# Performance work log

Measured on AMD Instinct MI355X. Metric: run time of the kernel, lower is better.

The kernel has to match this reference:

```python
import jax, jax.numpy as jnp
import numpy as np

D = 1024
H = 16
HD = D // H
T = 2048
B = 2
EPS = 1e-7

def setup_inputs() -> dict:
    key = jax.random.key(0)
    ks = jax.random.split(key, 16)
    s = 0.02
    return {
        "x":  jax.random.normal(ks[0], (B, T, D), jnp.float32),
        "Wq": jax.random.normal(ks[1], (D, D), jnp.float32) * s,
        "bq": jnp.zeros((D,), jnp.float32),
        "Wk": jax.random.normal(ks[2], (D, D), jnp.float32) * s,
        "bk": jnp.zeros((D,), jnp.float32),
        "Wv": jax.random.normal(ks[3], (D, D), jnp.float32) * s,
        "bv": jnp.zeros((D,), jnp.float32),
        "Wo": jax.random.normal(ks[4], (D, D), jnp.float32) * s,
        "bo": jnp.zeros((D,), jnp.float32),
        "W1": jax.random.normal(ks[5], (D, 4 * D), jnp.float32) * s,
        "b1": jnp.zeros((4 * D,), jnp.float32),
        "W2": jax.random.normal(ks[6], (4 * D, D), jnp.float32) * s,
        "b2": jnp.zeros((D,), jnp.float32),
        "g1": jnp.ones((D,), jnp.float32),
        "be1": jnp.zeros((D,), jnp.float32),
        "g2": jnp.ones((D,), jnp.float32),
        "be2": jnp.zeros((D,), jnp.float32),
    }

def layer_norm(x, gamma, beta):
    mu = jnp.mean(x, axis=-1, keepdims=True)
    var = jnp.mean(jnp.square(x - mu), axis=-1, keepdims=True)  # biased var
    return (x - mu) / jnp.sqrt(var + EPS) * gamma + beta

def attention(x, Wq, bq, Wk, bk, Wv, bv, Wo, bo):
    b, t, d = x.shape
    q = (x @ Wq + bq).reshape(b, t, H, HD).transpose(0, 2, 1, 3)  # [B,H,T,HD]
    k = (x @ Wk + bk).reshape(b, t, H, HD).transpose(0, 2, 1, 3)
    v = (x @ Wv + bv).reshape(b, t, H, HD).transpose(0, 2, 1, 3)
    scores = jnp.einsum("bhqd,bhkd->bhqk", q, k) / np.sqrt(HD).astype(np.float32)
    causal = jnp.tril(jnp.ones((t, t), bool))
    scores = jnp.where(causal, scores, -jnp.inf)
    attn = jax.nn.softmax(scores, axis=-1)
    out = jnp.einsum("bhqk,bhkd->bhqd", attn, v)
    out = out.transpose(0, 2, 1, 3).reshape(b, t, d)
    return out @ Wo + bo

def reference(x, Wq, bq, Wk, bk, Wv, bv, Wo, bo, W1, b1, W2, b2, g1, be1, g2, be2):
    x = x + attention(layer_norm(x, g1, be1), Wq, bq, Wk, bk, Wv, bv, Wo, bo)
    h = layer_norm(x, g2, be2)
    x = x + (jax.nn.relu(h @ W1 + b1) @ W2 + b2)
    return x
```

## Files before the change

kernel.cpp:

```cpp
#include <hip/hip_runtime.h>
#include <hip/hip_bf16.h>

#define Dm 1024
#define Hn 16
#define HDm 64
#define Tm 2048
#define Bm 2
#define MR (Bm*Tm)
#define SQK 3072

typedef __attribute__((ext_vector_type(8))) short bfrag8;
typedef __attribute__((ext_vector_type(4))) float floatx4;

__device__ __forceinline__ float bf2f(ushort u){
  union { unsigned int i; float f; } c; c.i = ((unsigned int)u)<<16; return c.f;
}
__device__ __forceinline__ ushort f2bf(float f){
  unsigned int u = __float_as_uint(f);
  u += 0x7fffu + ((u>>16)&1u);
  return (ushort)(u>>16);
}
__device__ __forceinline__ void gl2lds16(const ushort* g, ushort* l){
  __builtin_amdgcn_global_load_lds(
    (const __attribute__((address_space(1))) unsigned int*)g,
    (__attribute__((address_space(3))) unsigned int*)l,
    16, 0, 0);
}
__device__ __forceinline__ int is_f32(const unsigned int* g1w){
  return *g1w == 0x3F800000u;
}

#define POFF0 (1ul*524288)
#define POFF1 (9ul*524288)
#define POFF2 (25ul*524288)
#define POFF3 (73ul*524288)

__global__ __launch_bounds__(256) void prep_vec(const void* bq, const void* bk, const void* bv,
                                                const void* bo, const void* b1, const void* b2,
                                                const void* g1, const void* be1,
                                                const void* g2, const void* be2,
                                                float* __restrict__ dst){
  int i = blockIdx.x*256 + threadIdx.x;
  if (i >= 13312) return;
  int f = is_f32((const unsigned int*)g1);
  const void* src; int off;
  if      (i < 1024)  { src = bq;  off = i; }
  else if (i < 2048)  { src = bk;  off = i-1024; }
  else if (i < 3072)  { src = bv;  off = i-2048; }
  else if (i < 4096)  { src = bo;  off = i-3072; }
  else if (i < 8192)  { src = b1;  off = i-4096; }
  else if (i < 9216)  { src = b2;  off = i-8192; }
  else if (i < 10240) { src = g1;  off = i-9216; }
  else if (i < 11264) { src = be1; off = i-10240; }
  else if (i < 12288) { src = g2;  off = i-11264; }
  else                { src = be2; off = i-12288; }
  dst[i] = f ? ((const float*)src)[off] : bf2f(((const ushort*)src)[off]);
}

__device__ __forceinline__ void transpose_body(const void* src, ushort* dst,
                                               int K, int N, int f32){
  __shared__ ushort s[32][33];
  int bx = blockIdx.x, by = blockIdx.y;
  int tx = threadIdx.x, ty = threadIdx.y;
#pragma unroll
  for(int r=0;r<4;r++){
    size_t gi = (size_t)(by*32+ty+8*r)*N + bx*32+tx;
    s[ty+8*r][tx] = f32 ? f2bf(((const float*)src)[gi]) : ((const ushort*)src)[gi];
  }
  __syncthreads();
#pragma unroll
  for(int r=0;r<4;r++)
    dst[(size_t)(bx*32+ty+8*r)*K + by*32+tx] = s[tx][ty+8*r];
}
__global__ __launch_bounds__(256) void transpose_cast(const void* __restrict__ src,
                                                      ushort* __restrict__ dst,
                                                      int K, int N, const unsigned int* g1w){
  transpose_body(src, dst, K, N, is_f32(g1w));
}
__global__ __launch_bounds__(256) void transpose_qkvo(const void* Wq, const void* Wk,
                                                      const void* Wv, const void* Wo,
                                                      ushort* __restrict__ Wqkvt,
                                                      ushort* __restrict__ Wot,
                                                      const unsigned int* g1w){
  int z = blockIdx.z;
  const void* src = (z==0)?Wq:(z==1)?Wk:(z==2)?Wv:Wo;
  ushort* dst = (z<3) ? (Wqkvt + (size_t)z*1024*1024) : Wot;
  transpose_body(src, dst, 1024, 1024, is_f32(g1w));
}

__global__ __launch_bounds__(256) void vtrans(const ushort* __restrict__ qkv,
                                              ushort* __restrict__ vt){
  __shared__ ushort s[32][33];
  int bhz = blockIdx.z;
  int bx = blockIdx.x;
  int by = blockIdx.y;
  int tx = threadIdx.x, ty = threadIdx.y;
  int b = bhz>>4, h = bhz&15;
  const ushort* src = qkv + (size_t)b*Tm*SQK + 2048 + h*64;
#pragma unroll
  for(int r=0;r<4;r++)
    s[ty+8*r][tx] = src[(size_t)(bx*32+ty+8*r)*SQK + by*32+tx];
  __syncthreads();
  ushort* dst = vt + (size_t)bhz*HDm*Tm;
#pragma unroll
  for(int r=0;r<4;r++)
    dst[(size_t)(by*32+ty+8*r)*Tm + bx*32+tx] = s[tx][ty+8*r];
}

template<int MODE>
__global__ __launch_bounds__(256) void ln_kernel(const void* __restrict__ xin,
                                                 const float* __restrict__ g,
                                                 const float* __restrict__ be,
                                                 ushort* __restrict__ out,
                                                 const unsigned int* g1w){
  int row = blockIdx.x;
  int tid = threadIdx.x;
  size_t base = (size_t)row*Dm + tid*4;
  float v[4];
  bool f32in = (MODE==1) || (MODE==0 && is_f32(g1w));
  if (f32in){
    const float4 t = *(const float4*)((const float*)xin + base);
    v[0]=t.x; v[1]=t.y; v[2]=t.z; v[3]=t.w;
  } else {
    ushort4 t = *(const ushort4*)((const ushort*)xin + base);
    v[0]=bf2f(t.x); v[1]=bf2f(t.y); v[2]=bf2f(t.z); v[3]=bf2f(t.w);
  }
  float s  = v[0]+v[1]+v[2]+v[3];
  float s2 = v[0]*v[0]+v[1]*v[1]+v[2]*v[2]+v[3]*v[3];
#pragma unroll
  for(int o=1;o<64;o<<=1){
    s  += __shfl_xor(s,  o, 64);
    s2 += __shfl_xor(s2, o, 64);
  }
  __shared__ float red[8];
  int wv = tid>>6;
  if ((tid&63)==0){ red[wv]=s; red[wv+4]=s2; }
  __syncthreads();
  s  = red[0]+red[1]+red[2]+red[3];
  s2 = red[4]+red[5]+red[6]+red[7];
  float mu  = s  * (1.0f/Dm);
  float var = s2 * (1.0f/Dm) - mu*mu;
  float rstd = rsqrtf(var + 1e-7f);
  float4 gg = *(const float4*)(g  + tid*4);
  float4 bb = *(const float4*)(be + tid*4);
  ushort4 o4;
  o4.x = f2bf((v[0]-mu)*rstd*gg.x+bb.x);
  o4.y = f2bf((v[1]-mu)*rstd*gg.y+bb.y);
  o4.z = f2bf((v[2]-mu)*rstd*gg.z+bb.z);
  o4.w = f2bf((v[3]-mu)*rstd*gg.w+bb.w);
  *(ushort4*)(out + base) = o4;
}

#define BKt 64
enum { E_BF16=0, E_RELU=1, E_OPROJ=2, E_FINALB=3, E_PARTB=4, E_PARTB4=5 };

template<int EPI>
__global__ __launch_bounds__(512,2) void gemm256(const ushort* __restrict__ A, int lda,
                                                 const ushort* __restrict__ Bt, int ldb,
                                                 const float* __restrict__ bias,
                                                 void* __restrict__ Cout, int ldc,
                                                 int Ki,
                                                 const unsigned int* g1w){
  __shared__ ushort lds[65536];
  int tid = threadIdx.x;
  int lin = blockIdx.x;
  int xcd = lin&7, pos = lin>>3;
  int bm, bn, zid = 0;
  if (EPI==E_BF16){        bm=(xcd&3)*4+(pos&3);  bn=(xcd>>2)*6+(pos>>2); }
  else if (EPI==E_RELU){   bm=(xcd&3)*4+(pos&3);  bn=(xcd>>2)*8+(pos>>2); }
  else if (EPI==E_PARTB4){ zid=xcd>>1; bm=(xcd&1)*8+(pos>>2); bn=pos&3; }
  else {                   zid=xcd&1;  bm=(xcd>>1)*4+(pos>>2); bn=pos&3; }
  int wv = tid>>6, lane = tid&63;
  int quad = lane>>4, l16 = lane&15;
  int wm = (wv>>2)*128, wn = (wv&3)*64;
  int rl = lane>>3;
  int cs = ((lane&7)^rl)*8;
  const ushort* Aptr = A  + (size_t)bm*256*lda + (size_t)zid*Ki;
  const ushort* Bptr = Bt + (size_t)bn*256*ldb + (size_t)zid*Ki;
  floatx4 acc[8][4] = {};
  bfrag8 afr[4][2], bfr[4][2];
  const int NI = Ki>>7;

  auto STG = [&](ushort* dst, const ushort* g, int ld){
    gl2lds16(&g[(size_t)(wv*16+rl)*ld + cs],   dst + (wv*16)*64);
    gl2lds16(&g[(size_t)(wv*16+8+rl)*ld + cs], dst + (wv*16+8)*64);
  };
  auto LD8 = [&](const ushort* base, int r, int G)->bfrag8{
    return *(const bfrag8*)&base[r*64 + ((G ^ (r&7))<<3)];
  };
#define BAR256 __builtin_amdgcn_s_barrier()
#define LGKM0  do{ asm volatile("s_waitcnt lgkmcnt(0)" ::: "memory"); __builtin_amdgcn_sched_barrier(0);}while(0)
#define MM256(a_,b_,c_) c_ = __builtin_amdgcn_mfma_f32_16x16x32_bf16(a_,b_,c_,0,0,0)

  STG(lds+32768,      Bptr,                    ldb);
  STG(lds+32768+8192, Bptr+(size_t)128*ldb,    ldb);
  STG(lds,            Aptr,                    lda);
  STG(lds+8192,       Aptr+(size_t)128*lda,    lda);
  STG(lds+49152,      Bptr+64,                 ldb);
  STG(lds+49152+8192, Bptr+(size_t)128*ldb+64, ldb);
  STG(lds+16384,      Aptr+64,                 lda);
  asm volatile("s_waitcnt vmcnt(6)" ::: "memory");
  BAR256;

  for(int i=0;i<NI;i++){
    bool nl = (i < NI-1);
    int kc = i*128;
#pragma unroll
    for(int m=0;m<4;m++){ int r=wm+m*16+l16;
      afr[m][0]=LD8(lds, r, quad);  afr[m][1]=LD8(lds, r, 4|quad); }
#pragma unroll
    for(int j=0;j<4;j++){ int r=wn+j*16+l16;
      bfr[j][0]=LD8(lds+32768, r, quad); bfr[j][1]=LD8(lds+32768, r, 4|quad); }
    STG(lds+16384+8192, Aptr+(size_t)128*lda + kc+64, lda);
    BAR256; LGKM0;
    __builtin_amdgcn_s_setprio(1);
#pragma unroll
    for(int m=0;m<4;m++)
#pragma unroll
      for(int j=0;j<2;j++){ MM256(afr[m][0],bfr[j][0],acc[m][j]); MM256(afr[m][1],bfr[j][1],acc[m][j]); }
    __builtin_amdgcn_s_setprio(0);
    BAR256;
    if(nl) STG(lds+32768, Bptr + kc+128, ldb);
    BAR256;
    __builtin_amdgcn_s_setprio(1);
#pragma unroll
    for(int m=0;m<4;m++)
#pragma unroll
      for(int j=2;j<4;j++){ MM256(afr[m][0],bfr[j][0],acc[m][j]); MM256(afr[m][1],bfr[j][1],acc[m][j]); }
    __builtin_amdgcn_s_setprio(0);
    BAR256;
#pragma unroll
    for(int m=0;m<4;m++){ int r=wm+(4+m)*16+l16;
      afr[m][0]=LD8(lds, r, quad);  afr[m][1]=LD8(lds, r, 4|quad); }
    if(nl) STG(lds+32768+8192, Bptr+(size_t)128*ldb + kc+128, ldb);
    BAR256; LGKM0;
    __builtin_amdgcn_s_setprio(1);
#pragma unroll
    for(int m=0;m<4;m++)
#pragma unroll
      for(int j=2;j<4;j++){ MM256(afr[m][0],bfr[j][0],acc[4+m][j]); MM256(afr[m][1],bfr[j][1],acc[4+m][j]); }
    __builtin_amdgcn_s_setprio(0);
    BAR256;
    if(nl) STG(lds, Aptr + kc+128, lda);
    BAR256;
    __builtin_amdgcn_s_setprio(1);
#pragma unroll
    for(int m=0;m<4;m++)
#pragma unroll
      for(int j=0;j<2;j++){ MM256(afr[m][0],bfr[j][0],acc[4+m][j]); MM256(afr[m][1],bfr[j][1],acc[4+m][j]); }
    __builtin_amdgcn_s_setprio(0);
    if(nl) asm volatile("s_waitcnt vmcnt(6)" ::: "memory");
    else   asm volatile("s_waitcnt vmcnt(0)" ::: "memory");
    BAR256;
#pragma unroll
    for(int m=0;m<4;m++){ int r=wm+m*16+l16;
      afr[m][0]=LD8(lds+16384, r, quad);  afr[m][1]=LD8(lds+16384, r, 4|quad); }
#pragma unroll
    for(int j=0;j<4;j++){ int r=wn+j*16+l16;
      bfr[j][0]=LD8(lds+49152, r, quad); bfr[j][1]=LD8(lds+49152, r, 4|quad); }
    if(nl) STG(lds+8192, Aptr+(size_t)128*lda + kc+128, lda);
    BAR256; LGKM0;
    __builtin_amdgcn_s_setprio(1);
#pragma unroll
    for(int m=0;m<4;m++)
#pragma unroll
      for(int j=0;j<2;j++){ MM256(afr[m][0],bfr[j][0],acc[m][j]); MM256(afr[m][1],bfr[j][1],acc[m][j]); }
    __builtin_amdgcn_s_setprio(0);
    BAR256;
    if(nl) STG(lds+49152, Bptr + kc+192, ldb);
    BAR256;
    __builtin_amdgcn_s_setprio(1);
#pragma unroll
    for(int m=0;m<4;m++)
#pragma unroll
      for(int j=2;j<4;j++){ MM256(afr[m][0],bfr[j][0],acc[m][j]); MM256(afr[m][1],bfr[j][1],acc[m][j]); }
    __builtin_amdgcn_s_setprio(0);
    BAR256;
#pragma unroll
    for(int m=0;m<4;m++){ int r=wm+(4+m)*16+l16;
      afr[m][0]=LD8(lds+16384, r, quad);  afr[m][1]=LD8(lds+16384, r, 4|quad); }
    if(nl) STG(lds+49152+8192, Bptr+(size_t)128*ldb + kc+192, ldb);
    BAR256; LGKM0;
    __builtin_amdgcn_s_setprio(1);
#pragma unroll
    for(int m=0;m<4;m++)
#pragma unroll
      for(int j=2;j<4;j++){ MM256(afr[m][0],bfr[j][0],acc[4+m][j]); MM256(afr[m][1],bfr[j][1],acc[4+m][j]); }
    __builtin_amdgcn_s_setprio(0);
    BAR256;
    if(nl) STG(lds+16384, Aptr + kc+192, lda);
    BAR256;
    __builtin_amdgcn_s_setprio(1);
#pragma unroll
    for(int m=0;m<4;m++)
#pragma unroll
      for(int j=0;j<2;j++){ MM256(afr[m][0],bfr[j][0],acc[4+m][j]); MM256(afr[m][1],bfr[j][1],acc[4+m][j]); }
    __builtin_amdgcn_s_setprio(0);
    if(nl){ asm volatile("s_waitcnt vmcnt(6)" ::: "memory"); }
    BAR256;
  }

  ushort* part = (ushort*)Cout;
  if (EPI==E_PARTB)  part += (size_t)zid*MR*1024;
  if (EPI==E_PARTB4) part += (zid==0?POFF0 : zid==1?POFF1 : zid==2?POFF2 : POFF3);
#pragma unroll
  for(int i2=0;i2<8;i2++){
    int gr = bm*256 + wm + i2*16 + quad*4;
#pragma unroll
    for(int j=0;j<4;j++){
      int gc = bn*256 + wn + j*16 + l16;
      float bb = (EPI==E_PARTB || EPI==E_PARTB4) ? 0.0f : bias[gc];
#pragma unroll
      for(int rg=0; rg<4; rg++){
        size_t idx = (size_t)(gr+rg)*ldc + gc;
        float val = acc[i2][j][rg] + bb;
        if (EPI==E_RELU) part[idx] = f2bf(val>0.0f?val:0.0f);
        else             part[idx] = f2bf(val);
      }
    }
  }
#undef BAR256
#undef LGKM0
#undef MM256
}

__global__ __launch_bounds__(256) void ffn2_reduce(const ushort* __restrict__ p0,
                                                   const ushort* __restrict__ p1,
                                                   const float* __restrict__ bias,
                                                   const ushort* __restrict__ resid,
                                                   void* __restrict__ out,
                                                   const unsigned int* g1w){
  int e = (blockIdx.x*256 + threadIdx.x)*4;
  ushort4 a = *(const ushort4*)&p0[e];
  ushort4 b = *(const ushort4*)&p1[e];
  ushort4 r = *(const ushort4*)&resid[e];
  float4 bb = *(const float4*)&bias[e & 1023];
  float v0 = bf2f(a.x)+bf2f(b.x)+bb.x+bf2f(r.x);
  float v1 = bf2f(a.y)+bf2f(b.y)+bb.y+bf2f(r.y);
  float v2 = bf2f(a.z)+bf2f(b.z)+bb.z+bf2f(r.z);
  float v3 = bf2f(a.w)+bf2f(b.w)+bb.w+bf2f(r.w);
  if (is_f32(g1w)){
    float4 o = {v0,v1,v2,v3};
    *(float4*)((float*)out + e) = o;
  } else {
    ushort4 o = {f2bf(v0),f2bf(v1),f2bf(v2),f2bf(v3)};
    *(ushort4*)((ushort*)out + e) = o;
  }
}

__global__ __launch_bounds__(256) void ffn2_reduce4(const ushort* __restrict__ pb,
                                                    const float* __restrict__ bias,
                                                    const ushort* __restrict__ resid,
                                                    void* __restrict__ out,
                                                    const unsigned int* g1w){
  int e = (blockIdx.x*256 + threadIdx.x)*4;
  ushort4 a = *(const ushort4*)&pb[POFF0 + e];
  ushort4 b = *(const ushort4*)&pb[POFF1 + e];
  ushort4 c = *(const ushort4*)&pb[POFF2 + e];
  ushort4 d = *(const ushort4*)&pb[POFF3 + e];
  ushort4 r = *(const ushort4*)&resid[e];
  float4 bb = *(const float4*)&bias[e & 1023];
  float v0 = bf2f(a.x)+bf2f(b.x)+bf2f(c.x)+bf2f(d.x)+bb.x+bf2f(r.x);
  float v1 = bf2f(a.y)+bf2f(b.y)+bf2f(c.y)+bf2f(d.y)+bb.y+bf2f(r.y);
  float v2 = bf2f(a.z)+bf2f(b.z)+bf2f(c.z)+bf2f(d.z)+bb.z+bf2f(r.z);
  float v3 = bf2f(a.w)+bf2f(b.w)+bf2f(c.w)+bf2f(d.w)+bb.w+bf2f(r.w);
  if (is_f32(g1w)){
    float4 o = {v0,v1,v2,v3};
    *(float4*)((float*)out + e) = o;
  } else {
    ushort4 o = {f2bf(v0),f2bf(v1),f2bf(v2),f2bf(v3)};
    *(ushort4*)((ushort*)out + e) = o;
  }
}

template<int EPI>
__global__ __launch_bounds__(128) void gemm64_bt(const ushort* __restrict__ A, int lda,
                                                 const ushort* __restrict__ Bt, int ldb,
                                                 const float* __restrict__ bias,
                                                 const void*   __restrict__ resid,
                                                 void* __restrict__ Cout, int ldc,
                                                 int Ki,
                                                 const unsigned int* g1w){
  __shared__ ushort As[64*BKt];
  __shared__ ushort Bs[64*BKt];
  int tid = threadIdx.x;
  int id = blockIdx.x;
  int xcd = id&7, sdec = id>>3;
  int bn = sdec&15, bm = (sdec>>4)*8 + xcd;
  int wv = tid>>6, lane = tid&63;
  int quad = lane>>4, l16 = lane&15;
  int wm = wv*32;
  floatx4 acc[2][4] = {};
  const ushort* Aptr = A  + (size_t)bm*64*lda;
  const ushort* Bptr = Bt + (size_t)bn*64*ldb;
  int rl = lane>>3;
  int cs = ((lane&7) ^ rl)*8;

  for(int k0=0; k0<Ki; k0+=BKt){
    __syncthreads();
#pragma unroll
    for(int c=0;c<4;c++){
      gl2lds16(&Aptr[(size_t)(wv*32 + c*8 + rl)*lda + k0 + cs], &As[(wv*32 + c*8)*BKt]);
      gl2lds16(&Bptr[(size_t)(wv*32 + c*8 + rl)*ldb + k0 + cs], &Bs[(wv*32 + c*8)*BKt]);
    }
    __syncthreads();
#pragma unroll
    for(int f=0;f<2;f++){
      int sw = (((f<<2)|quad) ^ (l16&7))*8;
      bfrag8 a[2], b[4];
#pragma unroll
      for(int i=0;i<2;i++) a[i] = *(const bfrag8*)&As[(wm+i*16+l16)*BKt + sw];
#pragma unroll
      for(int j=0;j<4;j++) b[j] = *(const bfrag8*)&Bs[(j*16+l16)*BKt + sw];
#pragma unroll
      for(int i=0;i<2;i++)
#pragma unroll
        for(int j=0;j<4;j++)
          acc[i][j] = __builtin_amdgcn_mfma_f32_16x16x32_bf16(a[i], b[j], acc[i][j], 0,0,0);
    }
  }

  int f32 = is_f32(g1w);
#pragma unroll
  for(int i=0;i<2;i++){
    int gr = bm*64 + wm + i*16 + quad*4;
#pragma unroll
    for(int j=0;j<4;j++){
      int gc = bn*64 + j*16 + l16;
      float bb = bias[gc];
#pragma unroll
      for(int rg=0; rg<4; rg++){
        size_t idx = (size_t)(gr+rg)*ldc + gc;
        float val = acc[i][j][rg] + bb;
        if (EPI==E_OPROJ){
          float r = f32 ? ((const float*)resid)[idx] : bf2f(((const ushort*)resid)[idx]);
          ((ushort*)Cout)[idx] = f2bf(val + r);
        } else {
          float r = bf2f(((const ushort*)resid)[idx]);
          if (f32) ((float*)Cout)[idx] = val + r;
          else     ((ushort*)Cout)[idx] = f2bf(val + r);
        }
      }
    }
  }
}

#define PSTR2 72

__global__ __launch_bounds__(256) void attn_mfma(const ushort* __restrict__ qkv,
                                                 const ushort* __restrict__ vt,
                                                 ushort* __restrict__ out){
  __shared__ ushort Ks[64*64];
  __shared__ ushort Vs[64*64];
  __shared__ ushort Ps[64*PSTR2];
  int id = blockIdx.x;
  int xcd = id&7, s = id>>3;
  int cu = s&31, k = s>>5;
  int qt = (k&1) ? cu : 31-cu;
  int h = xcd + 8*(k&1), b = k>>1;
  int tid = threadIdx.x;
  int wv = tid>>6, lane = tid&63;
  int quad = lane>>4, l16 = lane&15;
  const ushort* qbase = qkv + (size_t)b*Tm*SQK + h*HDm;
  const ushort* kbase = qbase + Dm;
  const ushort* vtb   = vt + (size_t)(b*Hn+h)*HDm*Tm;
  size_t obase = (size_t)b*Tm*Dm + (size_t)h*HDm;
  int rl = lane>>3;
  int cs = ((lane&7) ^ rl)*8;

  int qrow = qt*64 + wv*16 + l16;
  bfrag8 aq[2];
#pragma unroll
  for(int f=0;f<2;f++){
    bfrag8 raw = *(const bfrag8*)&qbase[(size_t)qrow*SQK + f*32 + quad*8];
#pragma unroll
    for(int e=0;e<8;e++) aq[f][e] = (short)f2bf(bf2f((ushort)raw[e])*0.125f);
  }

  floatx4 oacc[4] = {};
  float lacc = 0.0f;
  int qglob = qt*64 + wv*16 + l16;
  int nr = qt + 1;

  for(int r=0; r<nr; r++){
    __syncthreads();
#pragma unroll
    for(int c=0;c<2;c++){
      int kr0 = wv*16 + c*8;
      gl2lds16(&kbase[(size_t)(r*64 + kr0 + rl)*SQK + cs], &Ks[kr0*64]);
      gl2lds16(&vtb[(size_t)(kr0 + rl)*Tm + r*64 + cs], &Vs[kr0*64]);
    }
    __syncthreads();

    floatx4 sv[4];
#pragma unroll
    for(int j=0;j<4;j++){
      int kr = j*16 + l16;
      int k7 = kr & 7;
      bfrag8 k0 = *(const bfrag8*)&Ks[kr*64 + ((quad     ^ k7)*8)];
      bfrag8 k1 = *(const bfrag8*)&Ks[kr*64 + (((4|quad) ^ k7)*8)];
      floatx4 z = {0.0f,0.0f,0.0f,0.0f};
      z = __builtin_amdgcn_mfma_f32_16x16x32_bf16(k0, aq[0], z, 0,0,0);
      z = __builtin_amdgcn_mfma_f32_16x16x32_bf16(k1, aq[1], z, 0,0,0);
      sv[j] = z;
    }
    if (r == qt){
#pragma unroll
      for(int j=0;j<4;j++){
        int gk0 = r*64 + j*16 + quad*4;
#pragma unroll
        for(int rg=0;rg<4;rg++)
          if (gk0 + rg > qglob) sv[j][rg] = -1.0e30f;
      }
    }

#pragma unroll
    for(int j=0;j<4;j++){
      float p0 = __expf(sv[j][0]);
      float p1 = __expf(sv[j][1]);
      float p2 = __expf(sv[j][2]);
      float p3 = __expf(sv[j][3]);
      lacc += (p0+p1)+(p2+p3);
      unsigned w0, w1;
      asm("v_cvt_pk_bf16_f32 %0, %1, %2" : "=v"(w0) : "v"(p0), "v"(p1));
      asm("v_cvt_pk_bf16_f32 %0, %1, %2" : "=v"(w1) : "v"(p2), "v"(p3));
      uint2 ww; ww.x = w0; ww.y = w1;
      *(uint2*)&Ps[(wv*16 + l16)*PSTR2 + j*16 + quad*4] = ww;
    }

    bfrag8 ap[2];
#pragma unroll
    for(int c=0;c<2;c++)
      ap[c] = *(const bfrag8*)&Ps[(wv*16 + l16)*PSTR2 + c*32 + quad*8];

#pragma unroll
    for(int j=0;j<4;j++){
      int dr = j*16 + l16;
      int d7 = dr & 7;
#pragma unroll
      for(int c=0;c<2;c++){
        bfrag8 bv = *(const bfrag8*)&Vs[dr*64 + (((c*4+quad) ^ d7)*8)];
        oacc[j] = __builtin_amdgcn_mfma_f32_16x16x32_bf16(ap[c], bv, oacc[j], 0,0,0);
      }
    }
  }

  lacc += __shfl_xor(lacc, 16, 64);
  lacc += __shfl_xor(lacc, 32, 64);
  float inv[4];
#pragma unroll
  for(int rg=0;rg<4;rg++){
    float den = __shfl(lacc, quad*4 + rg, 64);
    inv[rg] = 1.0f / den;
  }

#pragma unroll
  for(int j=0;j<4;j++)
#pragma unroll
    for(int rg=0;rg<4;rg++){
      int t = qt*64 + wv*16 + quad*4 + rg;
      out[obase + (size_t)t*Dm + j*16 + l16] = f2bf(oacc[j][rg] * inv[rg]);
    }
}

extern "C" void kernel_launch(void* const* d_in, const int* in_sizes, int n_in,
                              void* d_out, int out_size, void* d_ws, size_t ws_size,
                              hipStream_t stream) {
  const void* x   = d_in[0];
  const void* Wq  = d_in[1];
  const void* bq  = d_in[2];
  const void* Wk  = d_in[3];
  const void* bk  = d_in[4];
  const void* Wv  = d_in[5];
  const void* bv  = d_in[6];
  const void* Wo  = d_in[7];
  const void* bo  = d_in[8];
  const void* W1  = d_in[9];
  const void* b1  = d_in[10];
  const void* W2  = d_in[11];
  const void* b2  = d_in[12];
  const void* g1  = d_in[13];
  const void* be1 = d_in[14];
  const void* g2  = d_in[15];
  const void* be2 = d_in[16];
  const unsigned int* g1w = (const unsigned int*)g1;

  char* ws = (char*)d_ws;
  const size_t MB = 1024*1024;
  float*  biasf = (float*)(ws + 65536);
  ushort* Wqkvt = (ushort*)(ws + 1*MB);
  ushort* Wot   = (ushort*)(ws + 7*MB);
  ushort* W1t   = (ushort*)(ws + 9*MB);
  ushort* W2t   = (ushort*)(ws + 17*MB);
  ushort* p0    = (ushort*)(ws + 1*MB);
  ushort* p1    = (ushort*)(ws + 9*MB);
  ushort* ln1   = (ushort*)(ws + 25*MB);
  ushort* vtb   = (ushort*)(ws + 25*MB);
  ushort* h2    = (ushort*)(ws + 25*MB);
  ushort* qkv   = (ushort*)(ws + 33*MB);
  ushort* atb   = (ushort*)(ws + 57*MB);
  ushort* x1b   = (ushort*)(ws + 65*MB);
  ushort* h1    = (ushort*)(ws + 33*MB);

  prep_vec<<<52, 256, 0, stream>>>(bq,bk,bv,bo,b1,b2,g1,be1,g2,be2, biasf);

  dim3 tb(32,8);
  transpose_qkvo<<<dim3(32,32,4), tb, 0, stream>>>(Wq, Wk, Wv, Wo, Wqkvt, Wot, g1w);
  transpose_cast<<<dim3(128,32), tb, 0, stream>>>(W1, W1t, 1024, 4096, g1w);
  transpose_cast<<<dim3(32,128), tb, 0, stream>>>(W2, W2t, 4096, 1024, g1w);

  ln_kernel<0><<<MR, 256, 0, stream>>>(x, biasf+9216, biasf+10240, ln1, g1w);

  gemm256<E_BF16><<<192, 512, 0, stream>>>(ln1, 1024, Wqkvt, 1024, biasf, qkv, SQK, 1024, g1w);

  vtrans<<<dim3(64,2,32), tb, 0, stream>>>(qkv, vtb);

  attn_mfma<<<1024, 256, 0, stream>>>(qkv, vtb, atb);

  gemm64_bt<E_OPROJ><<<1024, 128, 0, stream>>>(atb, 1024, Wot, 1024, biasf+3072, x, x1b, 1024, 1024, g1w);

  ln_kernel<2><<<MR, 256, 0, stream>>>(x1b, biasf+11264, biasf+12288, h2, g1w);

  gemm256<E_RELU><<<256, 512, 0, stream>>>(h2, 1024, W1t, 1024, biasf+4096, h1, 4096, 1024, g1w);

  if (ws_size >= 82*MB){
    gemm256<E_PARTB4><<<256, 512, 0, stream>>>(h1, 4096, W2t, 4096, nullptr, d_ws, 1024, 1024, g1w);
    ffn2_reduce4<<<4096, 256, 0, stream>>>((const ushort*)d_ws, biasf+8192, x1b, d_out, g1w);
  } else {
    gemm256<E_PARTB><<<128, 512, 0, stream>>>(h1, 4096, W2t, 4096, nullptr, p0, 1024, 2048, g1w);
    ffn2_reduce<<<4096, 256, 0, stream>>>(p0, p1, biasf+8192, x1b, d_out, g1w);
  }
}
```

Before: 336.5 us.

## Split causal attention KV range across two blocks and combine partial sums

Each attention block now processes a pair of query tiles (p and 31-p), so every block gets a similar amount of causal work. The key/value tiles are split between two blocks by parity, which write unnormalized partial outputs and row denominators. A new combine kernel adds the two partials and normalizes them. This is meant to remove load imbalance and tail effects from the triangular causal workload, at the cost of an extra kernel launch, extra global traffic for the partials, and bf16 rounding of the unnormalized partial sums.

New measurement: 339.4 us. About the same (+0.9%).

```diff
diff --git a/kernel.cpp b/kernel.cpp
--- a/kernel.cpp
+++ b/kernel.cpp
@@ -449,15 +449,19 @@
 
 __global__ __launch_bounds__(256) void attn_mfma(const ushort* __restrict__ qkv,
                                                  const ushort* __restrict__ vt,
-                                                 ushort* __restrict__ out){
+                                                 ushort* __restrict__ pn0,
+                                                 ushort* __restrict__ pn1,
+                                                 float* __restrict__ den0,
+                                                 float* __restrict__ den1){
   __shared__ ushort Ks[64*64];
   __shared__ ushort Vs[64*64];
   __shared__ ushort Ps[64*PSTR2];
   int id = blockIdx.x;
   int xcd = id&7, s = id>>3;
-  int cu = s&31, k = s>>5;
-  int qt = (k&1) ? cu : 31-cu;
-  int h = xcd + 8*(k&1), b = k>>1;
+  int v = s>>6;
+  int hb = (s>>4)&3;
+  int p = s&15;
+  int h = xcd + 8*(hb&1), b = hb>>1;
   int tid = threadIdx.x;
   int wv = tid>>6, lane = tid&63;
   int quad = lane>>4, l16 = lane&15;
@@ -467,100 +471,124 @@
   size_t obase = (size_t)b*Tm*Dm + (size_t)h*HDm;
   int rl = lane>>3;
   int cs = ((lane&7) ^ rl)*8;
-
-  int qrow = qt*64 + wv*16 + l16;
-  bfrag8 aq[2];
-#pragma unroll
-  for(int f=0;f<2;f++){
-    bfrag8 raw = *(const bfrag8*)&qbase[(size_t)qrow*SQK + f*32 + quad*8];
-#pragma unroll
-    for(int e=0;e<8;e++) aq[f][e] = (short)f2bf(bf2f((ushort)raw[e])*0.125f);
-  }
-
-  floatx4 oacc[4] = {};
-  float lacc = 0.0f;
-  int qglob = qt*64 + wv*16 + l16;
-  int nr = qt + 1;
-
-  for(int r=0; r<nr; r++){
-    __syncthreads();
-#pragma unroll
-    for(int c=0;c<2;c++){
-      int kr0 = wv*16 + c*8;
-      gl2lds16(&kbase[(size_t)(r*64 + kr0 + rl)*SQK + cs], &Ks[kr0*64]);
-      gl2lds16(&vtb[(size_t)(kr0 + rl)*Tm + r*64 + cs], &Vs[kr0*64]);
+  ushort* pn = v ? pn1 : pn0;
+  float* den = v ? den1 : den0;
+
+  for(int tt=0; tt<2; tt++){
+    int qt = tt ? (31-p) : p;
+    int r0 = tt ? (1-v) : v;
+
+    int qrow = qt*64 + wv*16 + l16;
+    bfrag8 aq[2];
+#pragma unroll
+    for(int f=0;f<2;f++){
+      bfrag8 raw = *(const bfrag8*)&qbase[(size_t)qrow*SQK + f*32 + quad*8];
+#pragma unroll
+      for(int e=0;e<8;e++) aq[f][e] = (short)f2bf(bf2f((ushort)raw[e])*0.125f);
     }
-    __syncthreads();
-
-    floatx4 sv[4];
-#pragma unroll
-    for(int j=0;j<4;j++){
-      int kr = j*16 + l16;
-      int k7 = kr & 7;
-      bfrag8 k0 = *(const bfrag8*)&Ks[kr*64 + ((quad     ^ k7)*8)];
-      bfrag8 k1 = *(const bfrag8*)&Ks[kr*64 + (((4|quad) ^ k7)*8)];
-      floatx4 z = {0.0f,0.0f,0.0f,0.0f};
-      z = __builtin_amdgcn_mfma_f32_16x16x32_bf16(k0, aq[0], z, 0,0,0);
-      z = __builtin_amdgcn_mfma_f32_16x16x32_bf16(k1, aq[1], z, 0,0,0);
-      sv[j] = z;
+
+    floatx4 oacc[4] = {};
+    float lacc = 0.0f;
+    int qglob = qt*64 + wv*16 + l16;
+
+    for(int r=r0; r<=qt; r+=2){
+      __syncthreads();
+#pragma unroll
+      for(int c=0;c<2;c++){
+        int kr0 = wv*16 + c*8;
+        gl2lds16(&kbase[(size_t)(r*64 + kr0 + rl)*SQK + cs], &Ks[kr0*64]);
+        gl2lds16(&vtb[(size_t)(kr0 + rl)*Tm + r*64 + cs], &Vs[kr0*64]);
+      }
+      __syncthreads();
+
+      floatx4 sv[4];
+#pragma unroll
+      for(int j=0;j<4;j++){
+        int kr = j*16 + l16;
+        int k7 = kr & 7;
+        bfrag8 k0 = *(const bfrag8*)&Ks[kr*64 + ((quad     ^ k7)*8)];
+        bfrag8 k1 = *(const bfrag8*)&Ks[kr*64 + (((4|quad) ^ k7)*8)];
+        floatx4 z = {0.0f,0.0f,0.0f,0.0f};
+        z = __builtin_amdgcn_mfma_f32_16x16x32_bf16(k0, aq[0], z, 0,0,0);
+        z = __builtin_amdgcn_mfma_f32_16x16x32_bf16(k1, aq[1], z, 0,0,0);
+        sv[j] = z;
+      }
+      if (r == qt){
+#pragma unroll
+        for(int j=0;j<4;j++){
+          int gk0 = r*64 + j*16 + quad*4;
+#pragma unroll
+          for(int rg=0;rg<4;rg++)
+            if (gk0 + rg > qglob) sv[j][rg] = -1.0e30f;
+        }
+      }
+
+#pragma unroll
+      for(int j=0;j<4;j++){
+        float p0 = __expf(sv[j][0]);
+        float p1 = __expf(sv[j][1]);
+        float p2 = __expf(sv[j][2]);
+        float p3 = __expf(sv[j][3]);
+        lacc += (p0+p1)+(p2+p3);
+        unsigned w0, w1;
+        asm("v_cvt_pk_bf16_f32 %0, %1, %2" : "=v"(w0) : "v"(p0), "v"(p1));
+        asm("v_cvt_pk_bf16_f32 %0, %1, %2" : "=v"(w1) : "v"(p2), "v"(p3));
+        uint2 ww; ww.x = w0; ww.y = w1;
+        *(uint2*)&Ps[(wv*16 + l16)*PSTR2 + j*16 + quad*4] = ww;
+      }
+
+      bfrag8 ap[2];
+#pragma unroll
+      for(int c=0;c<2;c++)
+        ap[c] = *(const bfrag8*)&Ps[(wv*16 + l16)*PSTR2 + c*32 + quad*8];
+
+#pragma unroll
+      for(int j=0;j<4;j++){
+        int dr = j*16 + l16;
+        int d7 = dr & 7;
+#pragma unroll
+        for(int c=0;c<2;c++){
+          bfrag8 bv = *(const bfrag8*)&Vs[dr*64 + (((c*4+quad) ^ d7)*8)];
+          oacc[j] = __builtin_amdgcn_mfma_f32_16x16x32_bf16(ap[c], bv, oacc[j], 0,0,0);
+        }
+      }
     }
-    if (r == qt){
-#pragma unroll
-      for(int j=0;j<4;j++){
-        int gk0 = r*64 + j*16 + quad*4;
-#pragma unroll
-        for(int rg=0;rg<4;rg++)
-          if (gk0 + rg > qglob) sv[j][rg] = -1.0e30f;
-      }
-    }
-
-#pragma unroll
-    for(int j=0;j<4;j++){
-      float p0 = __expf(sv[j][0]);
-      float p1 = __expf(sv[j][1]);
-      float p2 = __expf(sv[j][2]);
-      float p3 = __expf(sv[j][3]);
-      lacc += (p0+p1)+(p2+p3);
-      unsigned w0, w1;
-      asm("v_cvt_pk_bf16_f32 %0, %1, %2" : "=v"(w0) : "v"(p0), "v"(p1));
-      asm("v_cvt_pk_bf16_f32 %0, %1, %2" : "=v"(w1) : "v"(p2), "v"(p3));
-      uint2 ww; ww.x = w0; ww.y = w1;
-      *(uint2*)&Ps[(wv*16 + l16)*PSTR2 + j*16 + quad*4] = ww;
-    }
-
-    bfrag8 ap[2];
-#pragma unroll
-    for(int c=0;c<2;c++)
-      ap[c] = *(const bfrag8*)&Ps[(wv*16 + l16)*PSTR2 + c*32 + quad*8];
-
-#pragma unroll
-    for(int j=0;j<4;j++){
-      int dr = j*16 + l16;
-      int d7 = dr & 7;
-#pragma unroll
-      for(int c=0;c<2;c++){
-        bfrag8 bv = *(const bfrag8*)&Vs[dr*64 + (((c*4+quad) ^ d7)*8)];
-        oacc[j] = __builtin_amdgcn_mfma_f32_16x16x32_bf16(ap[c], bv, oacc[j], 0,0,0);
-      }
-    }
-  }
-
-  lacc += __shfl_xor(lacc, 16, 64);
-  lacc += __shfl_xor(lacc, 32, 64);
-  float inv[4];
-#pragma unroll
-  for(int rg=0;rg<4;rg++){
-    float den = __shfl(lacc, quad*4 + rg, 64);
-    inv[rg] = 1.0f / den;
-  }
-
-#pragma unroll
-  for(int j=0;j<4;j++)
-#pragma unroll
-    for(int rg=0;rg<4;rg++){
-      int t = qt*64 + wv*16 + quad*4 + rg;
-      out[obase + (size_t)t*Dm + j*16 + l16] = f2bf(oacc[j][rg] * inv[rg]);
-    }
+
+    lacc += __shfl_xor(lacc, 16, 64);
+    lacc += __shfl_xor(lacc, 32, 64);
+    if (lane < 16)
+      den[(size_t)(b*Hn+h)*Tm + qt*64 + wv*16 + lane] = lacc;
+
+#pragma unroll
+    for(int j=0;j<4;j++)
+#pragma unroll
+      for(int rg=0;rg<4;rg++){
+        int t = qt*64 + wv*16 + quad*4 + rg;
+        pn[obase + (size_t)t*Dm + j*16 + l16] = f2bf(oacc[j][rg]);
+      }
+  }
+}
+
+__global__ __launch_bounds__(256) void attn_combine(const ushort* __restrict__ n1,
+                                                    const float* __restrict__ den0,
+                                                    const float* __restrict__ den1,
+                                                    ushort* __restrict__ n0out){
+  int e = (blockIdx.x*256 + threadIdx.x)*4;
+  int row = e >> 10;
+  int col = e & 1023;
+  int h = col >> 6;
+  int b = row >> 11;
+  int t = row & 2047;
+  size_t di = (size_t)(b*Hn+h)*Tm + t;
+  float inv = 1.0f / (den0[di] + den1[di]);
+  ushort4 a = *(const ushort4*)&n0out[e];
+  ushort4 c = *(const ushort4*)&n1[e];
+  ushort4 o;
+  o.x = f2bf((bf2f(a.x)+bf2f(c.x))*inv);
+  o.y = f2bf((bf2f(a.y)+bf2f(c.y))*inv);
+  o.z = f2bf((bf2f(a.z)+bf2f(c.z))*inv);
+  o.w = f2bf((bf2f(a.w)+bf2f(c.w))*inv);
+  *(ushort4*)&n0out[e] = o;
 }
 
 extern "C" void kernel_launch(void* const* d_in, const int* in_sizes, int n_in,
@@ -588,6 +616,8 @@
   char* ws = (char*)d_ws;
   const size_t MB = 1024*1024;
   float*  biasf = (float*)(ws + 65536);
+  float*  den0c = (float*)(ws + 256*1024);
+  float*  den1c = (float*)(ws + 512*1024);
   ushort* Wqkvt = (ushort*)(ws + 1*MB);
   ushort* Wot   = (ushort*)(ws + 7*MB);
   ushort* W1t   = (ushort*)(ws + 9*MB);
@@ -599,6 +629,7 @@
   ushort* h2    = (ushort*)(ws + 25*MB);
   ushort* qkv   = (ushort*)(ws + 33*MB);
   ushort* atb   = (ushort*)(ws + 57*MB);
+  ushort* pn1b  = (ushort*)(ws + 65*MB);
   ushort* x1b   = (ushort*)(ws + 65*MB);
   ushort* h1    = (ushort*)(ws + 33*MB);
 
@@ -615,7 +646,8 @@
 
   vtrans<<<dim3(64,2,32), tb, 0, stream>>>(qkv, vtb);
 
-  attn_mfma<<<1024, 256, 0, stream>>>(qkv, vtb, atb);
+  attn_mfma<<<1024, 256, 0, stream>>>(qkv, vtb, atb, pn1b, den0c, den1c);
+  attn_combine<<<4096, 256, 0, stream>>>(pn1b, den0c, den1c, atb);
 
   gemm64_bt<E_OPROJ><<<1024, 128, 0, stream>>>(atb, 1024, Wot, 1024, biasf+3072, x, x1b, 1024, 1024, g1w);
 
```
